# Kernel tuning notes

Hardware: AMD Instinct MI355X
Metric: run time of the kernel (lower is better)

Reference implementation:

```python
import jax, jax.numpy as jnp
import numpy as np

N_NODES = 10000
N_EDGES = 160000
C_IN, C_HID, C_OUT = 16, 16, 16
IN_ORDER = HID_ORDER = OUT_ORDER = 2
BAND_LIMIT = 2
N_RINGS = 2
NUM_SAMPLES = 7
N_FREQ = 2 * BAND_LIMIT + 1  # 5


def _transport(x_e, phi, order):
    """Parallel-transport source features along edges: rotate order-m (cos,sin)
    pairs (components 2m-1, 2m) by angle m*phi. x_e: [E,C,2*order+1], phi: [E]."""
    comps = [x_e[:, :, 0:1]]
    for m in range(1, order + 1):
        c = jnp.cos(m * phi)[:, None]
        s = jnp.sin(m * phi)[:, None]
        a = x_e[:, :, 2 * m - 1]
        b = x_e[:, :, 2 * m]
        comps.append(jnp.stack([c * a - s * b, s * a + c * b], axis=-1).reshape(x_e.shape[0], x_e.shape[1], 2))
    return jnp.concatenate(comps, axis=-1)


def _gem_conv(x, src, dst, precomp, phi, W, Ws, b, in_order, num_nodes):
    """Gauge-equivariant conv: gather source feats, transport, contract with the
    per-edge angular/radial basis and kernel weights, scatter-sum to targets,
    plus a self-interaction and an equivariant (order-0) bias.
    x: [N,Cin,Qi]; precomp: [E,F,R]; W: [Cout,Cin,Qo,Qi,F,R]; Ws: [Cout,Cin,Qo,Qi]; b: [Cout]."""
    xt = _transport(x[src], phi, in_order)                    # [E,Cin,Qi]
    msg = jnp.einsum('ecq,efr,ocpqfr->eop', xt, precomp, W)   # [E,Cout,Qo]
    agg = jax.ops.segment_sum(msg, dst, num_segments=num_nodes)
    y = agg + jnp.einsum('ncq,ocpq->nop', x, Ws)
    return y.at[:, :, 0].add(b)


def _regular_nonlin(x, order, num_samples):
    """Fourier -> regular samples -> ReLU -> Fourier. Exact for num_samples >= 2*order+1."""
    K = num_samples
    theta = (2.0 * np.pi / K) * jnp.arange(K, dtype=x.dtype)          # [K]
    m = jnp.arange(1, order + 1, dtype=x.dtype)                        # [order]
    ang = theta[:, None] * m[None, :]                                  # [K,order]
    cs = jnp.stack([jnp.cos(ang), jnp.sin(ang)], axis=-1).reshape(K, 2 * order)
    B = jnp.concatenate([jnp.ones((K, 1), x.dtype), cs], axis=1)      # [K, 2*order+1]
    scale = jnp.concatenate([jnp.full((1,), 1.0 / K, x.dtype),
                             jnp.full((2 * order,), 2.0 / K, x.dtype)])
    s = jnp.maximum(jnp.einsum('ncp,kp->nck', x, B), 0.0)             # ReLU in regular rep
    return jnp.einsum('nck,kp->ncp', s, B) * scale


def setup_inputs() -> dict:
    key = jax.random.key(0)
    ks = jax.random.split(key, 12)
    Qi, Qh, Qo = 2 * IN_ORDER + 1, 2 * HID_ORDER + 1, 2 * OUT_ORDER + 1
    sc = 0.1
    return {
        'x': jax.random.normal(ks[0], (N_NODES, C_IN, Qi), jnp.float32),
        'edge_index': jax.random.randint(ks[1], (N_EDGES, 2), 0, N_NODES, jnp.int64),
        'precomp_neigh_edge': jax.random.uniform(ks[2], (N_EDGES, N_FREQ, N_RINGS), jnp.float32),
        'connection': jax.random.normal(ks[3], (N_EDGES,), jnp.float32),
        'W1': sc * jax.random.normal(ks[4], (C_HID, C_IN, Qh, Qi, N_FREQ, N_RINGS), jnp.float32),
        'b1': sc * jax.random.normal(ks[5], (C_HID,), jnp.float32),
        'Ws1': sc * jax.random.normal(ks[6], (C_HID, C_IN, Qh, Qi), jnp.float32),
        'W2': sc * jax.random.normal(ks[7], (C_OUT, C_HID, Qo, Qh, N_FREQ, N_RINGS), jnp.float32),
        'b2': sc * jax.random.normal(ks[8], (C_OUT,), jnp.float32),
        'Ws2': sc * jax.random.normal(ks[9], (C_OUT, C_HID, Qo, Qh), jnp.float32),
    }


def reference(x, edge_index, precomp_neigh_edge, connection, W1, b1, Ws1, W2, b2, Ws2):
    src = edge_index[:, 0]
    dst = edge_index[:, 1]
    y = _gem_conv(x, src, dst, precomp_neigh_edge, connection, W1, Ws1, b1, IN_ORDER, N_NODES)
    y = _regular_nonlin(y, HID_ORDER, NUM_SAMPLES)  # regular_non_lin=True
    y = _gem_conv(y, src, dst, precomp_neigh_edge, connection, W2, Ws2, b2, HID_ORDER, N_NODES)
    o = min(y.shape[2], x.shape[2])  # residual (lin = Identity since in_ch == out_ch)
    y = y.at[:, :, :o].add(x[:, :, :o])
    return _regular_nonlin(y, OUT_ORDER, NUM_SAMPLES)  # final_activation=True
```

## Files before the change

kernel.cpp:

```cpp
#include <hip/hip_runtime.h>
#include <hip/hip_bf16.h>
#include <hip/hip_fp16.h>
#include <math.h>

#ifndef M_PI
#define M_PI 3.14159265358979323846
#endif

#define NN 10000
#define NE 160000
#define NC 16
#define NQ 5
#define NFR 10
#define CQ 80
#define OP 80

#define MAXDEG 64

#define KTOT2 896
#define KS 28
#define WTN 71680
#define APAD 936
#define NPB 8

typedef __attribute__((ext_vector_type(8))) _Float16 f16x8;
typedef __attribute__((ext_vector_type(4))) float f32x4;

static __device__ __forceinline__ unsigned short f2h_u(float f) {
    return __builtin_bit_cast(unsigned short, (_Float16)f);
}
static __device__ __forceinline__ unsigned pack2h(float lo, float hi) {
    return (unsigned)f2h_u(lo) | ((unsigned)f2h_u(hi) << 16);
}
#define RFL(x) __builtin_amdgcn_readfirstlane(x)

__global__ void prep_all(const int* __restrict__ ei, const float* __restrict__ phi,
                         const float* __restrict__ pre,
                         const float* __restrict__ W1, const float* __restrict__ Ws1,
                         const float* __restrict__ W2, const float* __restrict__ Ws2,
                         int* __restrict__ cnt, int* __restrict__ srcs,
                         float4* __restrict__ recs,
                         unsigned short* __restrict__ Wt1, unsigned short* __restrict__ Wt2) {
    int i = blockIdx.x * blockDim.x + threadIdx.x;
    if (i < NE) {
        const int dst  = ei[2 * i + 1];
        const int srcn = ei[2 * i];
        const int rank = atomicAdd(&cnt[dst], 1);
        if (rank < MAXDEG) {
            float s1, c1;
            sincosf(phi[i], &s1, &c1);
            const float* tp = pre + (size_t)i * NFR;
            const int slot = dst * MAXDEG + rank;
            float4* rp = recs + (size_t)slot * 3;
            rp[0] = make_float4(tp[0], tp[1], tp[2], tp[3]);
            rp[1] = make_float4(tp[4], tp[5], tp[6], tp[7]);
            rp[2] = make_float4(tp[8], tp[9], c1, s1);
            srcs[slot] = srcn;
        }
    }
    if (i < WTN) {
        int j    = i & 7;
        int lane = (i >> 3) & 63;
        int grp  = i >> 9;
        int ks   = grp / 5;
        int nt   = grp % 5;
        int quad = lane >> 4;
        int lrow = lane & 15;
        int n    = 16 * nt + lrow;
        int k    = 32 * ks + 8 * quad + j;
        int o = n / 5, p = n % 5;
        float v1, v2;
        if (k < 800) {
            int cq = k / 10, fr = k % 10;
            int c = cq / 5, q = cq % 5;
            int f = fr >> 1, r = fr & 1;
            int src = ((((o * NC + c) * NQ + p) * NQ + q) * 5 + f) * 2 + r;
            v1 = W1[src]; v2 = W2[src];
        } else if (k < 880) {
            int cq = k - 800;
            int c = cq / 5, q = cq % 5;
            int src = ((o * NC + c) * NQ + p) * NQ + q;
            v1 = Ws1[src]; v2 = Ws2[src];
        } else {
            v1 = 0.0f; v2 = 0.0f;
        }
        Wt1[i] = f2h_u(v1); Wt2[i] = f2h_u(v2);
    }
}

__global__ __launch_bounds__(512)
void layer_fused(const float* __restrict__ xin, const int* __restrict__ srcs,
                 const float4* __restrict__ recs, const int* __restrict__ cnt,
                 const unsigned short* __restrict__ Wt, const float* __restrict__ b,
                 const float* __restrict__ res,
                 float* __restrict__ outp) {
    __shared__ __align__(16) unsigned short A_s[NPB * APAD];
    __shared__ float y_s[NPB * OP];

    const int tid = threadIdx.x;
    const int n0 = blockIdx.x * NPB;
    const int wid = RFL(tid >> 6);
    const int lane = tid & 63;
    const int n = n0 + wid;

    const int l48 = (lane < 48) ? lane : 0;
    const int c   = l48 / 3;
    const int g   = l48 - 3 * c;
    const int cqA = 5 * c + ((g == 0) ? 0 : (g == 1) ? 1 : 3);
    const int cqB = cqA + 1;
    const bool hi = (g == 2);

    const int base = n * MAXDEG;
    int deg = RFL(cnt[n]);
    if (deg > MAXDEG) deg = MAXDEG;

    float accA[10], accB[10];
    #pragma unroll
    for (int f = 0; f < 10; ++f) { accA[f] = 0.f; accB[f] = 0.f; }

#define EDGE_FMA(r0, r1, r2, xa, xb)                                          \
    do {                                                                      \
        const float c1 = (r2).z, s1 = (r2).w;                                 \
        const float c2 = c1 * c1 - s1 * s1;                                   \
        const float s2 = 2.0f * c1 * s1;                                      \
        const float cs = hi ? c2 : c1;                                        \
        const float sn = hi ? s2 : s1;                                        \
        const float xtA = (g == 0) ? (xa) : (cs * (xa) - sn * (xb));          \
        const float xtB = sn * (xa) + cs * (xb);                              \
        accA[0] += xtA * (r0).x;  accB[0] += xtB * (r0).x;                    \
        accA[1] += xtA * (r0).y;  accB[1] += xtB * (r0).y;                    \
        accA[2] += xtA * (r0).z;  accB[2] += xtB * (r0).z;                    \
        accA[3] += xtA * (r0).w;  accB[3] += xtB * (r0).w;                    \
        accA[4] += xtA * (r1).x;  accB[4] += xtB * (r1).x;                    \
        accA[5] += xtA * (r1).y;  accB[5] += xtB * (r1).y;                    \
        accA[6] += xtA * (r1).z;  accB[6] += xtB * (r1).z;                    \
        accA[7] += xtA * (r1).w;  accB[7] += xtB * (r1).w;                    \
        accA[8] += xtA * (r2).x;  accB[8] += xtB * (r2).x;                    \
        accA[9] += xtA * (r2).y;  accB[9] += xtB * (r2).y;                    \
    } while (0)

    if (deg > 0) {
        #define SLOT(i) (base + (((i) < deg) ? (i) : (deg - 1)))
        int sA0 = RFL(srcs[SLOT(0)]);
        int sB0 = RFL(srcs[SLOT(1)]);
        int sA1 = RFL(srcs[SLOT(2)]);
        int sB1 = RFL(srcs[SLOT(3)]);
        const float4* p;
        p = recs + (size_t)SLOT(0) * 3; float4 rA0a = p[0], rA0b = p[1], rA0c = p[2];
        p = recs + (size_t)SLOT(1) * 3; float4 rB0a = p[0], rB0b = p[1], rB0c = p[2];
        p = recs + (size_t)SLOT(2) * 3; float4 rA1a = p[0], rA1b = p[1], rA1c = p[2];
        p = recs + (size_t)SLOT(3) * 3; float4 rB1a = p[0], rB1b = p[1], rB1c = p[2];
        const float* xr;
        xr = xin + (size_t)sA0 * CQ; float xaA = xr[cqA], xbA = xr[cqB];
        xr = xin + (size_t)sB0 * CQ; float xaB = xr[cqA], xbB = xr[cqB];

        int i = 0;
        for (; i + 2 <= deg; i += 2) {
            const int nsA = RFL(srcs[SLOT(i + 4)]);
            const int nsB = RFL(srcs[SLOT(i + 5)]);
            const float* x1 = xin + (size_t)sA1 * CQ;
            const float* x2 = xin + (size_t)sB1 * CQ;
            const float nxaA = x1[cqA], nxbA = x1[cqB];
            const float nxaB = x2[cqA], nxbB = x2[cqB];
            const float4* q1 = recs + (size_t)SLOT(i + 4) * 3;
            const float4* q2 = recs + (size_t)SLOT(i + 5) * 3;
            const float4 nrAa = q1[0], nrAb = q1[1], nrAc = q1[2];
            const float4 nrBa = q2[0], nrBb = q2[1], nrBc = q2[2];
            EDGE_FMA(rA0a, rA0b, rA0c, xaA, xbA);
            EDGE_FMA(rB0a, rB0b, rB0c, xaB, xbB);
            sA0 = sA1; sB0 = sB1; sA1 = nsA; sB1 = nsB;
            xaA = nxaA; xbA = nxbA; xaB = nxaB; xbB = nxbB;
            rA0a = rA1a; rA0b = rA1b; rA0c = rA1c;
            rB0a = rB1a; rB0b = rB1b; rB0c = rB1c;
            rA1a = nrAa; rA1b = nrAb; rA1c = nrAc;
            rB1a = nrBa; rB1b = nrBb; rB1c = nrBc;
        }
        if (deg & 1) {
            EDGE_FMA(rA0a, rA0b, rA0c, xaA, xbA);
        }
        #undef SLOT
    }
#undef EDGE_FMA

    if (lane < 48) {
        unsigned* awA = (unsigned*)&A_s[wid * APAD + cqA * 10];
        awA[0] = pack2h(accA[0], accA[1]);
        awA[1] = pack2h(accA[2], accA[3]);
        awA[2] = pack2h(accA[4], accA[5]);
        awA[3] = pack2h(accA[6], accA[7]);
        awA[4] = pack2h(accA[8], accA[9]);
        A_s[wid * APAD + 800 + cqA] = f2h_u(xin[(size_t)n * CQ + cqA]);
        if (g != 0) {
            unsigned* awB = (unsigned*)&A_s[wid * APAD + cqB * 10];
            awB[0] = pack2h(accB[0], accB[1]);
            awB[1] = pack2h(accB[2], accB[3]);
            awB[2] = pack2h(accB[4], accB[5]);
            awB[3] = pack2h(accB[6], accB[7]);
            awB[4] = pack2h(accB[8], accB[9]);
            A_s[wid * APAD + 800 + cqB] = f2h_u(xin[(size_t)n * CQ + cqB]);
        }
    }
    if (lane < 16) A_s[wid * APAD + 880 + lane] = 0;

    __syncthreads();

    if (tid < 320) {
        const int nt = tid >> 6, lq = tid & 63;
        const int lrow = lq & 15, quad = lq >> 4;
        const int arow = lrow & 7;
        const f16x8* __restrict__ wf = (const f16x8*)Wt;
        f32x4 acc = (f32x4){0.f, 0.f, 0.f, 0.f};
        #pragma unroll 4
        for (int ks = 0; ks < KS; ++ks) {
            f16x8 bfrag = wf[(ks * 5 + nt) * 64 + lq];
            f16x8 a = *(const f16x8*)(&A_s[arow * APAD + 32 * ks + 8 * quad]);
            acc = __builtin_amdgcn_mfma_f32_16x16x32_f16(a, bfrag, acc, 0, 0, 0);
        }
        const int op = 16 * nt + lrow;
        const float bias = (op % 5 == 0) ? b[op / 5] : 0.0f;
        if (quad < 2) {
            #pragma unroll
            for (int r = 0; r < 4; ++r)
                y_s[(quad * 4 + r) * OP + op] = acc[r] + bias;
        }
    }
    __syncthreads();

    if (tid < 128) {
        const int nl = tid >> 4;
        const int ch = tid & 15;
        const float* vp = &y_s[nl * OP + ch * 5];
        float a0 = vp[0], a1 = vp[1], a2 = vp[2], a3 = vp[3], a4 = vp[4];
        if (res != nullptr) {
            const float* rp = res + (size_t)(n0 + nl) * CQ + ch * 5;
            a0 += rp[0]; a1 += rp[1]; a2 += rp[2]; a3 += rp[3]; a4 += rp[4];
        }
        float o0 = 0.f, o1 = 0.f, o2 = 0.f, o3 = 0.f, o4 = 0.f;
        #pragma unroll
        for (int k = 0; k < 7; ++k) {
            float th = (float)(2.0 * M_PI / 7.0) * (float)k;
            float c1k = cosf(th), s1k = sinf(th);
            float c2k = cosf(2.0f * th), s2k = sinf(2.0f * th);
            float s = a0 + a1 * c1k + a2 * s1k + a3 * c2k + a4 * s2k;
            s = fmaxf(s, 0.0f);
            o0 += s;
            o1 += s * c1k; o2 += s * s1k;
            o3 += s * c2k; o4 += s * s2k;
        }
        const float i7 = 1.0f / 7.0f, t7 = 2.0f / 7.0f;
        float* po = outp + (size_t)(n0 + nl) * OP + ch * 5;
        po[0] = o0 * i7;
        po[1] = o1 * t7; po[2] = o2 * t7;
        po[3] = o3 * t7; po[4] = o4 * t7;
    }
}

extern "C" void kernel_launch(void* const* d_in, const int* in_sizes, int n_in,
                              void* d_out, int out_size, void* d_ws, size_t ws_size,
                              hipStream_t stream) {
    const float* x    = (const float*)d_in[0];
    const int*   ei   = (const int*)d_in[1];
    const float* pre  = (const float*)d_in[2];
    const float* phi  = (const float*)d_in[3];
    const float* W1   = (const float*)d_in[4];
    const float* b1   = (const float*)d_in[5];
    const float* Ws1  = (const float*)d_in[6];
    const float* W2   = (const float*)d_in[7];
    const float* b2   = (const float*)d_in[8];
    const float* Ws2  = (const float*)d_in[9];
    float* out = (float*)d_out;

    unsigned short* Wt1 = (unsigned short*)d_ws;
    unsigned short* Wt2 = Wt1 + WTN;
    float* h  = (float*)(Wt2 + WTN);
    float4* recs = (float4*)(h + (size_t)NN * OP);
    int* srcs   = (int*)(recs + (size_t)NN * MAXDEG * 3);
    int* cnt    = srcs + (size_t)NN * MAXDEG;

    hipMemsetAsync(cnt, 0, NN * sizeof(int), stream);
    prep_all<<<(NE + 255) / 256, 256, 0, stream>>>(ei, phi, pre, W1, Ws1, W2, Ws2,
                                                   cnt, srcs, recs, Wt1, Wt2);
    layer_fused<<<NN / NPB, 512, 0, stream>>>(x, srcs, recs, cnt, Wt1, b1, nullptr, h);
    layer_fused<<<NN / NPB, 512, 0, stream>>>(h, srcs, recs, cnt, Wt2, b2, x, out);
}
```

Before: 145.5 us.

## Split each node's edge loop across two waves with LDS partial reduction

```diff
diff --git a/kernel.cpp b/kernel.cpp
--- a/kernel.cpp
+++ b/kernel.cpp
@@ -21,7 +21,8 @@
 #define KS 28
 #define WTN 71680
 #define APAD 936
-#define NPB 8
+#define NPB 4
+#define PPAD 21
 
 typedef __attribute__((ext_vector_type(8))) _Float16 f16x8;
 typedef __attribute__((ext_vector_type(4))) float f32x4;
@@ -95,13 +96,16 @@
                  const float* __restrict__ res,
                  float* __restrict__ outp) {
     __shared__ __align__(16) unsigned short A_s[NPB * APAD];
+    __shared__ float part_s[NPB][64][PPAD];
     __shared__ float y_s[NPB * OP];
 
     const int tid = threadIdx.x;
     const int n0 = blockIdx.x * NPB;
     const int wid = RFL(tid >> 6);
     const int lane = tid & 63;
-    const int n = n0 + wid;
+    const int nl   = wid >> 1;
+    const int half = wid & 1;
+    const int n = n0 + nl;
 
     const int l48 = (lane < 48) ? lane : 0;
     const int c   = l48 / 3;
@@ -113,6 +117,13 @@
     const int base = n * MAXDEG;
     int deg = RFL(cnt[n]);
     if (deg > MAXDEG) deg = MAXDEG;
+
+    const int h   = (deg + 1) >> 1;
+    const int loE = half ? h : 0;
+    const int cntE = (half ? deg : h) - loE;
+
+    const float xselfA = xin[(size_t)n * CQ + cqA];
+    const float xselfB = xin[(size_t)n * CQ + cqB];
 
     float accA[10], accB[10];
     #pragma unroll
@@ -139,8 +150,8 @@
         accA[9] += xtA * (r2).y;  accB[9] += xtB * (r2).y;                    \
     } while (0)
 
-    if (deg > 0) {
-        #define SLOT(i) (base + (((i) < deg) ? (i) : (deg - 1)))
+    if (cntE > 0) {
+        #define SLOT(i) (base + loE + (((i) < cntE) ? (i) : (cntE - 1)))
         int sA0 = RFL(srcs[SLOT(0)]);
         int sB0 = RFL(srcs[SLOT(1)]);
         int sA1 = RFL(srcs[SLOT(2)]);
@@ -155,7 +166,7 @@
         xr = xin + (size_t)sB0 * CQ; float xaB = xr[cqA], xbB = xr[cqB];
 
         int i = 0;
-        for (; i + 2 <= deg; i += 2) {
+        for (; i + 2 <= cntE; i += 2) {
             const int nsA = RFL(srcs[SLOT(i + 4)]);
             const int nsB = RFL(srcs[SLOT(i + 5)]);
             const float* x1 = xin + (size_t)sA1 * CQ;
@@ -175,39 +186,51 @@
             rA1a = nrAa; rA1b = nrAb; rA1c = nrAc;
             rB1a = nrBa; rB1b = nrBb; rB1c = nrBc;
         }
-        if (deg & 1) {
+        if (cntE & 1) {
             EDGE_FMA(rA0a, rA0b, rA0c, xaA, xbA);
         }
         #undef SLOT
     }
 #undef EDGE_FMA
 
-    if (lane < 48) {
-        unsigned* awA = (unsigned*)&A_s[wid * APAD + cqA * 10];
-        awA[0] = pack2h(accA[0], accA[1]);
-        awA[1] = pack2h(accA[2], accA[3]);
-        awA[2] = pack2h(accA[4], accA[5]);
-        awA[3] = pack2h(accA[6], accA[7]);
-        awA[4] = pack2h(accA[8], accA[9]);
-        A_s[wid * APAD + 800 + cqA] = f2h_u(xin[(size_t)n * CQ + cqA]);
-        if (g != 0) {
-            unsigned* awB = (unsigned*)&A_s[wid * APAD + cqB * 10];
-            awB[0] = pack2h(accB[0], accB[1]);
-            awB[1] = pack2h(accB[2], accB[3]);
-            awB[2] = pack2h(accB[4], accB[5]);
-            awB[3] = pack2h(accB[6], accB[7]);
-            awB[4] = pack2h(accB[8], accB[9]);
-            A_s[wid * APAD + 800 + cqB] = f2h_u(xin[(size_t)n * CQ + cqB]);
-        }
-    }
-    if (lane < 16) A_s[wid * APAD + 880 + lane] = 0;
-
+    if (half == 1) {
+        float* pp = &part_s[nl][lane][0];
+        #pragma unroll
+        for (int j = 0; j < 10; ++j) { pp[j] = accA[j]; pp[10 + j] = accB[j]; }
+    }
+    __syncthreads();
+
+    if (half == 0) {
+        const float* pp = &part_s[nl][lane][0];
+        #pragma unroll
+        for (int j = 0; j < 10; ++j) { accA[j] += pp[j]; accB[j] += pp[10 + j]; }
+
+        if (lane < 48) {
+            unsigned* awA = (unsigned*)&A_s[nl * APAD + cqA * 10];
+            awA[0] = pack2h(accA[0], accA[1]);
+            awA[1] = pack2h(accA[2], accA[3]);
+            awA[2] = pack2h(accA[4], accA[5]);
+            awA[3] = pack2h(accA[6], accA[7]);
+            awA[4] = pack2h(accA[8], accA[9]);
+            A_s[nl * APAD + 800 + cqA] = f2h_u(xselfA);
+            if (g != 0) {
+                unsigned* awB = (unsigned*)&A_s[nl * APAD + cqB * 10];
+                awB[0] = pack2h(accB[0], accB[1]);
+                awB[1] = pack2h(accB[2], accB[3]);
+                awB[2] = pack2h(accB[4], accB[5]);
+                awB[3] = pack2h(accB[6], accB[7]);
+                awB[4] = pack2h(accB[8], accB[9]);
+                A_s[nl * APAD + 800 + cqB] = f2h_u(xselfB);
+            }
+        }
+        if (lane < 16) A_s[nl * APAD + 880 + lane] = 0;
+    }
     __syncthreads();
 
     if (tid < 320) {
         const int nt = tid >> 6, lq = tid & 63;
         const int lrow = lq & 15, quad = lq >> 4;
-        const int arow = lrow & 7;
+        const int arow = lrow & 3;
         const f16x8* __restrict__ wf = (const f16x8*)Wt;
         f32x4 acc = (f32x4){0.f, 0.f, 0.f, 0.f};
         #pragma unroll 4
@@ -218,21 +241,21 @@
         }
         const int op = 16 * nt + lrow;
         const float bias = (op % 5 == 0) ? b[op / 5] : 0.0f;
-        if (quad < 2) {
+        if (quad == 0) {
             #pragma unroll
             for (int r = 0; r < 4; ++r)
-                y_s[(quad * 4 + r) * OP + op] = acc[r] + bias;
+                y_s[r * OP + op] = acc[r] + bias;
         }
     }
     __syncthreads();
 
-    if (tid < 128) {
-        const int nl = tid >> 4;
-        const int ch = tid & 15;
-        const float* vp = &y_s[nl * OP + ch * 5];
+    if (tid < 64) {
+        const int nle = tid >> 4;
+        const int ch  = tid & 15;
+        const float* vp = &y_s[nle * OP + ch * 5];
         float a0 = vp[0], a1 = vp[1], a2 = vp[2], a3 = vp[3], a4 = vp[4];
         if (res != nullptr) {
-            const float* rp = res + (size_t)(n0 + nl) * CQ + ch * 5;
+            const float* rp = res + (size_t)(n0 + nle) * CQ + ch * 5;
             a0 += rp[0]; a1 += rp[1]; a2 += rp[2]; a3 += rp[3]; a4 += rp[4];
         }
         float o0 = 0.f, o1 = 0.f, o2 = 0.f, o3 = 0.f, o4 = 0.f;
@@ -248,7 +271,7 @@
             o3 += s * c2k; o4 += s * s2k;
         }
         const float i7 = 1.0f / 7.0f, t7 = 2.0f / 7.0f;
-        float* po = outp + (size_t)(n0 + nl) * OP + ch * 5;
+        float* po = outp + (size_t)(n0 + nle) * OP + ch * 5;
         po[0] = o0 * i7;
         po[1] = o1 * t7; po[2] = o2 * t7;
         po[3] = o3 * t7; po[4] = o4 * t7;
```

Measured after the change: 150.7 us. 1.04x slower.
